# Performance work log

Measured on AMD Instinct MI355X. Metric: run time of the kernel, lower is better.

## Reference

```python
import jax, jax.numpy as jnp
import numpy as np

N, E, D, DE = 40000, 640000, 128, 64
LAMDA = 0.5
NEG_SLOPE = 0.01  # F.leaky_relu default


def setup_inputs() -> dict:
    key = jax.random.key(0)
    ks = jax.random.split(key, 8)
    node_h = jax.random.normal(ks[0], (N, D), dtype=jnp.float32)
    edge_h = jax.random.normal(ks[1], (E, DE), dtype=jnp.float32)
    src = jax.random.randint(ks[2], (E,), 0, N)
    dst = jax.random.randint(ks[3], (E,), 0, N)
    # parameters (torch Linear layout: [out, in])
    fc_w = jax.random.normal(ks[4], (D, D), dtype=jnp.float32) / np.sqrt(D)
    edge_fc_w = jax.random.normal(ks[5], (DE, DE), dtype=jnp.float32) / np.sqrt(DE)
    edge_fc_b = jax.random.normal(ks[6], (DE,), dtype=jnp.float32) * 0.01
    attn_w = jax.random.normal(ks[7], (1, 2 * D + DE), dtype=jnp.float32) / np.sqrt(2 * D + DE)
    return {"node_h": node_h, "edge_h": edge_h, "src": src, "dst": dst,
            "fc_w": fc_w, "edge_fc_w": edge_fc_w, "edge_fc_b": edge_fc_b, "attn_w": attn_w}


def reference(node_h, edge_h, src, dst, fc_w, edge_fc_w, edge_fc_b, attn_w):
    n = node_h.shape[0]
    z = node_h @ fc_w.T                       # [N, D]
    edge_z = edge_h @ edge_fc_w.T + edge_fc_b  # [E, DE]
    # attn_fc(concat([z_src, z_dst, edge_z])) == z_src@w_s + z_dst@w_d + edge_z@w_e
    w = attn_w[0]
    w_s, w_d, w_e = w[:D], w[D:2 * D], w[2 * D:]
    s_node = z @ w_s                           # [N]
    d_node = z @ w_d                           # [N]
    e = s_node[src] + d_node[dst] + edge_z @ w_e  # [E]
    e = jax.nn.leaky_relu(e, NEG_SLOPE)
    # segment softmax over incoming edges of each dst node
    m = jax.ops.segment_max(e, dst, num_segments=n)          # [N]
    ex = jnp.exp(e - m[dst])                                  # [E]
    denom = jax.ops.segment_sum(ex, dst, num_segments=n)     # [N]
    alpha = ex / denom[dst]                                   # [E]
    h = jax.ops.segment_sum(alpha[:, None] * z[src], dst, num_segments=n)  # [N, D]
    return (1.0 - LAMDA) * node_h + LAMDA * h
```

## Files before the change

### kernel.cpp

```cpp
#include <hip/hip_runtime.h>

#define NNODE 40000
#define NEDGE 640000
#define DD 128
#define DE 64
#define SCAN_NBLK ((NNODE + 255) / 256)

#define NODE_BLOCKS 1024
#define EDGE_BLOCKS 4096
#define FUSED_GRID (NODE_BLOCKS + EDGE_BLOCKS)

typedef float fvec4 __attribute__((ext_vector_type(4)));

__device__ __forceinline__ unsigned short f2bf(float f) {
    union { float f; unsigned int i; } c; c.f = f;
    unsigned int b = c.i;
    return (unsigned short)((b + 0x7fffu + ((b >> 16) & 1u)) >> 16);
}

__global__ __launch_bounds__(256) void fused_a(
        const float* __restrict__ node_h,
        const float* __restrict__ fc_w,
        const float* __restrict__ attw,
        const float* __restrict__ efw,
        const float* __restrict__ efb,
        const float* __restrict__ edge_h,
        unsigned int* __restrict__ z_bf,
        float* __restrict__ s_node,
        float* __restrict__ d_node,
        float* __restrict__ ez,
        int* __restrict__ deg) {
    int t = threadIdx.x;
    int b = blockIdx.x;

    int zi = b * 256 + t;
    if (zi < NNODE) deg[zi] = 0;

    if ((b % 5) != 0) {
        int eb = b - b / 5 - 1;
        __shared__ float v[DE + 1];
        if (t < DE) {
            float acc = 0.f;
            for (int j = 0; j < DE; ++j)
                acc += efw[j * DE + t] * attw[2 * DD + j];
            v[t] = acc;
        } else if (t == DE) {
            float acc = 0.f;
            for (int j = 0; j < DE; ++j)
                acc += efb[j] * attw[2 * DD + j];
            v[DE] = acc;
        }
        __syncthreads();

        int lane = t & 63;
        int wave = t >> 6;
        int sub  = lane & 7;
        const float* vv = &v[8 * sub];
        int ebase = eb * 32 + wave * 8 + (lane >> 3);

        for (int e = ebase; e < NEDGE; e += EDGE_BLOCKS * 32) {
            const fvec4* eh = (const fvec4*)(edge_h + (size_t)e * DE);
            fvec4 u0 = __builtin_nontemporal_load(eh + 2 * sub);
            fvec4 u1 = __builtin_nontemporal_load(eh + 2 * sub + 1);
            float ezv = u0.x * vv[0] + u0.y * vv[1] + u0.z * vv[2] + u0.w * vv[3]
                      + u1.x * vv[4] + u1.y * vv[5] + u1.z * vv[6] + u1.w * vv[7];
            ezv += __shfl_xor(ezv, 1, 64);
            ezv += __shfl_xor(ezv, 2, 64);
            ezv += __shfl_xor(ezv, 4, 64);
            if (sub == 0) ez[e] = ezv + v[DE];
        }
        return;
    }

    int nblk = b / 5;
    int th = t & 127, half = t >> 7;

    float4 wreg[DD / 4];
    const float4* wr = (const float4*)(fc_w + th * DD);
#pragma unroll
    for (int i = 0; i < DD / 4; ++i) wreg[i] = wr[i];
    float ws_att = attw[th];
    float wd_att = attw[DD + th];

    __shared__ float x[2][DD];
    __shared__ float red_s[4], red_d[4];

    for (int nb = nblk * 2; nb < NNODE; nb += NODE_BLOCKS * 2) {
        int n = nb + half;
        __syncthreads();
        x[half][th] = node_h[(size_t)n * DD + th];
        __syncthreads();
        const float4* xv = (const float4*)x[half];
        float acc = 0.f;
#pragma unroll
        for (int i = 0; i < DD / 4; ++i) {
            float4 a = wreg[i];
            float4 bx = xv[i];
            acc += a.x * bx.x + a.y * bx.y + a.z * bx.z + a.w * bx.w;
        }
        float nxt = __shfl_down(acc, 1, 64);
        if ((th & 1) == 0) {
            unsigned int p = (unsigned int)f2bf(acc) |
                             ((unsigned int)f2bf(nxt) << 16);
            z_bf[(size_t)n * (DD / 2) + (th >> 1)] = p;
        }

        float sv = acc * ws_att;
        float dv = acc * wd_att;
#pragma unroll
        for (int off = 32; off > 0; off >>= 1) {
            sv += __shfl_down(sv, off, 64);
            dv += __shfl_down(dv, off, 64);
        }
        int wv = t >> 6;
        if ((t & 63) == 0) { red_s[wv] = sv; red_d[wv] = dv; }
        __syncthreads();
        if (t == 0) {
            s_node[nb]     = red_s[0] + red_s[1];
            d_node[nb]     = red_d[0] + red_d[1];
        }
        if (t == 128) {
            s_node[nb + 1] = red_s[2] + red_s[3];
            d_node[nb + 1] = red_d[2] + red_d[3];
        }
    }
}

__global__ __launch_bounds__(256) void pass1b(
        const int* __restrict__ src,
        const int* __restrict__ dst,
        const float* __restrict__ s_node,
        const float* __restrict__ d_node,
        const float* __restrict__ ez,
        float* __restrict__ ex,
        int* __restrict__ deg) {
    int e = blockIdx.x * 256 + threadIdx.x;
    if (e >= NEDGE) return;
    int s = src[e], d = dst[e];
    float ev = s_node[s] + d_node[d] + ez[e];
    ev = ev > 0.f ? ev : 0.01f * ev;
    ex[e] = __expf(ev);
    atomicAdd(&deg[d], 1);
}

__global__ __launch_bounds__(256) void scan_a(const int* __restrict__ deg,
                                              int* __restrict__ lscan,
                                              int* __restrict__ blocksum) {
    __shared__ int s[256];
    int t = threadIdx.x;
    int idx = blockIdx.x * 256 + t;
    int v = (idx < NNODE) ? deg[idx] : 0;
    s[t] = v;
    __syncthreads();
    for (int off = 1; off < 256; off <<= 1) {
        int add = (t >= off) ? s[t - off] : 0;
        __syncthreads();
        s[t] += add;
        __syncthreads();
    }
    if (idx < NNODE) lscan[idx] = s[t] - v;
    if (t == 255) blocksum[blockIdx.x] = s[255];
}

__global__ __launch_bounds__(256) void scan_c(const int* __restrict__ lscan,
                                              const int* __restrict__ blocksum,
                                              int* __restrict__ rowstart,
                                              int* __restrict__ poscnt) {
    __shared__ int s[256];
    int t = threadIdx.x;
    int v = (t < SCAN_NBLK) ? blocksum[t] : 0;
    s[t] = v;
    __syncthreads();
    for (int off = 1; off < 256; off <<= 1) {
        int add = (t >= off) ? s[t - off] : 0;
        __syncthreads();
        s[t] += add;
        __syncthreads();
    }
    __shared__ int excl[256];
    excl[t] = s[t] - v;
    __syncthreads();

    int idx = blockIdx.x * 256 + t;
    if (idx < NNODE) {
        int r = lscan[idx] + excl[blockIdx.x];
        rowstart[idx] = r;
        poscnt[idx]   = r;
    }
    if (blockIdx.x == 0 && t == 0) rowstart[NNODE] = s[255];
}

__global__ void edge_pass2(const int* __restrict__ src,
                           const int* __restrict__ dst,
                           const float* __restrict__ ex,
                           int* __restrict__ poscnt,
                           int2* __restrict__ se_s) {
    int e = blockIdx.x * blockDim.x + threadIdx.x;
    if (e >= NEDGE) return;
    int d = dst[e];
    int p = atomicAdd(&poscnt[d], 1);
    se_s[p] = make_int2(src[e], __float_as_int(ex[e]));
}

__device__ __forceinline__ void acc8(float* a, uint4 w, float ex) {
    a[0] += ex * __uint_as_float(w.x << 16);
    a[1] += ex * __uint_as_float(w.x & 0xffff0000u);
    a[2] += ex * __uint_as_float(w.y << 16);
    a[3] += ex * __uint_as_float(w.y & 0xffff0000u);
    a[4] += ex * __uint_as_float(w.z << 16);
    a[5] += ex * __uint_as_float(w.z & 0xffff0000u);
    a[6] += ex * __uint_as_float(w.w << 16);
    a[7] += ex * __uint_as_float(w.w & 0xffff0000u);
}

__global__ __launch_bounds__(256) void gather_kernel(
        const float* __restrict__ node_h,
        const uint4* __restrict__ z_bf,
        const int* __restrict__ rowstart,
        const int2* __restrict__ se_s,
        float* __restrict__ out) {
    int wave = threadIdx.x >> 6;
    int lane = threadIdx.x & 63;
    int quarter = lane >> 4;
    int hl = lane & 15;
    int n = blockIdx.x * 4 + wave;
    if (n >= NNODE) return;

    int beg = rowstart[n];
    int end = rowstart[n + 1];

    float a[8] = {0.f, 0.f, 0.f, 0.f, 0.f, 0.f, 0.f, 0.f};
    float den = 0.f;
    int j = beg + quarter;
    for (; j + 12 < end; j += 16) {
        int2 se0 = se_s[j];
        int2 se1 = se_s[j + 4];
        int2 se2 = se_s[j + 8];
        int2 se3 = se_s[j + 12];
        uint4 w0 = z_bf[(size_t)se0.x * 16 + hl];
        uint4 w1 = z_bf[(size_t)se1.x * 16 + hl];
        uint4 w2 = z_bf[(size_t)se2.x * 16 + hl];
        uint4 w3 = z_bf[(size_t)se3.x * 16 + hl];
        float ex0 = __int_as_float(se0.y);
        float ex1 = __int_as_float(se1.y);
        float ex2 = __int_as_float(se2.y);
        float ex3 = __int_as_float(se3.y);
        acc8(a, w0, ex0);
        acc8(a, w1, ex1);
        acc8(a, w2, ex2);
        acc8(a, w3, ex3);
        den += (ex0 + ex1) + (ex2 + ex3);
    }
    for (; j + 4 < end; j += 8) {
        int2 se0 = se_s[j];
        int2 se1 = se_s[j + 4];
        uint4 w0 = z_bf[(size_t)se0.x * 16 + hl];
        uint4 w1 = z_bf[(size_t)se1.x * 16 + hl];
        float ex0 = __int_as_float(se0.y);
        float ex1 = __int_as_float(se1.y);
        acc8(a, w0, ex0);
        acc8(a, w1, ex1);
        den += ex0 + ex1;
    }
    if (j < end) {
        int2 se = se_s[j];
        uint4 w = z_bf[(size_t)se.x * 16 + hl];
        float ex = __int_as_float(se.y);
        acc8(a, w, ex);
        den += ex;
    }

#pragma unroll
    for (int k = 0; k < 8; ++k) {
        a[k] += __shfl_xor(a[k], 16, 64);
        a[k] += __shfl_xor(a[k], 32, 64);
    }
    den += __shfl_xor(den, 16, 64);
    den += __shfl_xor(den, 32, 64);

    if (quarter == 0) {
        float inv = den > 0.f ? 0.5f / den : 0.f;
        size_t o = (size_t)n * (DD / 4) + 2 * hl;
        fvec4 nh0 = ((const fvec4*)node_h)[o];
        fvec4 nh1 = ((const fvec4*)node_h)[o + 1];
        fvec4 r0, r1;
        r0.x = 0.5f * nh0.x + a[0] * inv;
        r0.y = 0.5f * nh0.y + a[1] * inv;
        r0.z = 0.5f * nh0.z + a[2] * inv;
        r0.w = 0.5f * nh0.w + a[3] * inv;
        r1.x = 0.5f * nh1.x + a[4] * inv;
        r1.y = 0.5f * nh1.y + a[5] * inv;
        r1.z = 0.5f * nh1.z + a[6] * inv;
        r1.w = 0.5f * nh1.w + a[7] * inv;
        __builtin_nontemporal_store(r0, (fvec4*)out + o);
        __builtin_nontemporal_store(r1, (fvec4*)out + o + 1);
    }
}

extern "C" void kernel_launch(void* const* d_in, const int* in_sizes, int n_in,
                              void* d_out, int out_size, void* d_ws, size_t ws_size,
                              hipStream_t stream) {
    const float* node_h    = (const float*)d_in[0];
    const float* edge_h    = (const float*)d_in[1];
    const int*   src       = (const int*)d_in[2];
    const int*   dst       = (const int*)d_in[3];
    const float* fc_w      = (const float*)d_in[4];
    const float* edge_fc_w = (const float*)d_in[5];
    const float* edge_fc_b = (const float*)d_in[6];
    const float* attn_w    = (const float*)d_in[7];
    float* out = (float*)d_out;

    char* ws = (char*)d_ws;
    unsigned int* z_bf = (unsigned int*)ws;
    int2*  se_s     = (int2*)(ws + (size_t)NNODE * 64 * 4);
    float* s_node   = (float*)(se_s + NEDGE);
    float* d_node   = s_node + NNODE;
    float* ez       = d_node + NNODE;
    float* ex       = ez + NEDGE;
    int*   deg      = (int*)(ex + NEDGE);
    int*   lscan    = deg + NNODE;
    int*   blocksum = lscan + NNODE;
    int*   rowstart = blocksum + 256;
    int*   poscnt   = rowstart + NNODE + 1;

    fused_a<<<FUSED_GRID, 256, 0, stream>>>(node_h, fc_w, attn_w, edge_fc_w,
                                            edge_fc_b, edge_h, z_bf, s_node,
                                            d_node, ez, deg);
    pass1b<<<(NEDGE + 255) / 256, 256, 0, stream>>>(src, dst, s_node, d_node,
                                                    ez, ex, deg);
    scan_a<<<SCAN_NBLK, 256, 0, stream>>>(deg, lscan, blocksum);
    scan_c<<<SCAN_NBLK, 256, 0, stream>>>(lscan, blocksum, rowstart, poscnt);
    edge_pass2<<<NEDGE / 256, 256, 0, stream>>>(src, dst, ex, poscnt, se_s);
    gather_kernel<<<NNODE / 4, 256, 0, stream>>>(node_h, (const uint4*)z_bf,
                                                 rowstart, se_s, out);
}
```

Measured before the change: 420.5 us.

## Split fused node/edge kernel, fold degree count and exp into edge passes

Replaces the interleaved node/edge fused kernel with a dedicated node projection kernel (128 threads, two nodes per iteration) and a separate edge-projection kernel. The edge kernel also does the degree atomics. The leaky-relu/exp score computation moves into the scatter pass, removing the separate pass1b kernel and the intermediate ex array round trip. In exchange, node and edge work no longer overlap within one launch, and the scatter pass now does random gathers of s_node/d_node before its atomics.

```diff
diff --git a/kernel.cpp b/kernel.cpp
--- a/kernel.cpp
+++ b/kernel.cpp
@@ -6,10 +6,6 @@
 #define DE 64
 #define SCAN_NBLK ((NNODE + 255) / 256)
 
-#define NODE_BLOCKS 1024
-#define EDGE_BLOCKS 4096
-#define FUSED_GRID (NODE_BLOCKS + EDGE_BLOCKS)
-
 typedef float fvec4 __attribute__((ext_vector_type(4)));
 
 __device__ __forceinline__ unsigned short f2bf(float f) {
@@ -18,129 +14,141 @@
     return (unsigned short)((b + 0x7fffu + ((b >> 16) & 1u)) >> 16);
 }
 
-__global__ __launch_bounds__(256) void fused_a(
+__global__ __launch_bounds__(128) void node_z(
         const float* __restrict__ node_h,
         const float* __restrict__ fc_w,
         const float* __restrict__ attw,
         const float* __restrict__ efw,
         const float* __restrict__ efb,
-        const float* __restrict__ edge_h,
         unsigned int* __restrict__ z_bf,
         float* __restrict__ s_node,
         float* __restrict__ d_node,
-        float* __restrict__ ez,
+        float* __restrict__ vc,
         int* __restrict__ deg) {
     int t = threadIdx.x;
-    int b = blockIdx.x;
-
-    int zi = b * 256 + t;
+
+    int zi = blockIdx.x * 128 + t;
     if (zi < NNODE) deg[zi] = 0;
 
-    if ((b % 5) != 0) {
-        int eb = b - b / 5 - 1;
-        __shared__ float v[DE + 1];
+    if (blockIdx.x == 0) {
         if (t < DE) {
             float acc = 0.f;
             for (int j = 0; j < DE; ++j)
                 acc += efw[j * DE + t] * attw[2 * DD + j];
-            v[t] = acc;
-        } else if (t == DE) {
+            vc[t] = acc;
+        }
+        if (t == 0) {
             float acc = 0.f;
             for (int j = 0; j < DE; ++j)
                 acc += efb[j] * attw[2 * DD + j];
-            v[DE] = acc;
-        }
-        __syncthreads();
-
-        int lane = t & 63;
-        int wave = t >> 6;
-        int sub  = lane & 7;
-        const float* vv = &v[8 * sub];
-        int ebase = eb * 32 + wave * 8 + (lane >> 3);
-
-        for (int e = ebase; e < NEDGE; e += EDGE_BLOCKS * 32) {
-            const fvec4* eh = (const fvec4*)(edge_h + (size_t)e * DE);
-            fvec4 u0 = __builtin_nontemporal_load(eh + 2 * sub);
-            fvec4 u1 = __builtin_nontemporal_load(eh + 2 * sub + 1);
-            float ezv = u0.x * vv[0] + u0.y * vv[1] + u0.z * vv[2] + u0.w * vv[3]
-                      + u1.x * vv[4] + u1.y * vv[5] + u1.z * vv[6] + u1.w * vv[7];
-            ezv += __shfl_xor(ezv, 1, 64);
-            ezv += __shfl_xor(ezv, 2, 64);
-            ezv += __shfl_xor(ezv, 4, 64);
-            if (sub == 0) ez[e] = ezv + v[DE];
-        }
-        return;
-    }
-
-    int nblk = b / 5;
-    int th = t & 127, half = t >> 7;
+            vc[DE] = acc;
+        }
+    }
 
     float4 wreg[DD / 4];
-    const float4* wr = (const float4*)(fc_w + th * DD);
+    const float4* wr = (const float4*)(fc_w + t * DD);
 #pragma unroll
     for (int i = 0; i < DD / 4; ++i) wreg[i] = wr[i];
-    float ws_att = attw[th];
-    float wd_att = attw[DD + th];
-
-    __shared__ float x[2][DD];
-    __shared__ float red_s[4], red_d[4];
-
-    for (int nb = nblk * 2; nb < NNODE; nb += NODE_BLOCKS * 2) {
-        int n = nb + half;
-        __syncthreads();
-        x[half][th] = node_h[(size_t)n * DD + th];
-        __syncthreads();
-        const float4* xv = (const float4*)x[half];
-        float acc = 0.f;
+    float ws_att = attw[t];
+    float wd_att = attw[DD + t];
+
+    __shared__ float x0[DD], x1[DD];
+    __shared__ float red[4][2];
+
+    for (int nb = blockIdx.x * 2; nb < NNODE; nb += 2048) {
+        __syncthreads();
+        x0[t] = node_h[(size_t)nb * DD + t];
+        x1[t] = node_h[(size_t)(nb + 1) * DD + t];
+        __syncthreads();
+        const float4* xv0 = (const float4*)x0;
+        const float4* xv1 = (const float4*)x1;
+        float acc0 = 0.f, acc1 = 0.f;
 #pragma unroll
         for (int i = 0; i < DD / 4; ++i) {
             float4 a = wreg[i];
-            float4 bx = xv[i];
-            acc += a.x * bx.x + a.y * bx.y + a.z * bx.z + a.w * bx.w;
-        }
-        float nxt = __shfl_down(acc, 1, 64);
-        if ((th & 1) == 0) {
-            unsigned int p = (unsigned int)f2bf(acc) |
-                             ((unsigned int)f2bf(nxt) << 16);
-            z_bf[(size_t)n * (DD / 2) + (th >> 1)] = p;
-        }
-
-        float sv = acc * ws_att;
-        float dv = acc * wd_att;
+            float4 b0 = xv0[i];
+            float4 b1 = xv1[i];
+            acc0 += a.x * b0.x + a.y * b0.y + a.z * b0.z + a.w * b0.w;
+            acc1 += a.x * b1.x + a.y * b1.y + a.z * b1.z + a.w * b1.w;
+        }
+        float nxt0 = __shfl_down(acc0, 1, 64);
+        float nxt1 = __shfl_down(acc1, 1, 64);
+        if ((t & 1) == 0) {
+            unsigned int p0 = (unsigned int)f2bf(acc0) |
+                              ((unsigned int)f2bf(nxt0) << 16);
+            unsigned int p1 = (unsigned int)f2bf(acc1) |
+                              ((unsigned int)f2bf(nxt1) << 16);
+            z_bf[(size_t)nb * (DD / 2) + (t >> 1)]       = p0;
+            z_bf[(size_t)(nb + 1) * (DD / 2) + (t >> 1)] = p1;
+        }
+
+        float s0 = acc0 * ws_att, d0 = acc0 * wd_att;
+        float s1 = acc1 * ws_att, d1 = acc1 * wd_att;
 #pragma unroll
         for (int off = 32; off > 0; off >>= 1) {
-            sv += __shfl_down(sv, off, 64);
-            dv += __shfl_down(dv, off, 64);
+            s0 += __shfl_down(s0, off, 64);
+            d0 += __shfl_down(d0, off, 64);
+            s1 += __shfl_down(s1, off, 64);
+            d1 += __shfl_down(d1, off, 64);
         }
         int wv = t >> 6;
-        if ((t & 63) == 0) { red_s[wv] = sv; red_d[wv] = dv; }
+        if ((t & 63) == 0) {
+            red[0][wv] = s0; red[1][wv] = d0;
+            red[2][wv] = s1; red[3][wv] = d1;
+        }
         __syncthreads();
         if (t == 0) {
-            s_node[nb]     = red_s[0] + red_s[1];
-            d_node[nb]     = red_d[0] + red_d[1];
-        }
-        if (t == 128) {
-            s_node[nb + 1] = red_s[2] + red_s[3];
-            d_node[nb + 1] = red_d[2] + red_d[3];
-        }
-    }
-}
-
-__global__ __launch_bounds__(256) void pass1b(
-        const int* __restrict__ src,
+            s_node[nb]     = red[0][0] + red[0][1];
+            d_node[nb]     = red[1][0] + red[1][1];
+            s_node[nb + 1] = red[2][0] + red[2][1];
+            d_node[nb + 1] = red[3][0] + red[3][1];
+        }
+    }
+}
+
+__global__ __launch_bounds__(256) void edge_ez(
+        const float* __restrict__ edge_h,
+        const float* __restrict__ vc,
         const int* __restrict__ dst,
-        const float* __restrict__ s_node,
-        const float* __restrict__ d_node,
-        const float* __restrict__ ez,
-        float* __restrict__ ex,
+        float* __restrict__ ez,
         int* __restrict__ deg) {
-    int e = blockIdx.x * 256 + threadIdx.x;
-    if (e >= NEDGE) return;
-    int s = src[e], d = dst[e];
-    float ev = s_node[s] + d_node[d] + ez[e];
-    ev = ev > 0.f ? ev : 0.01f * ev;
-    ex[e] = __expf(ev);
-    atomicAdd(&deg[d], 1);
+    __shared__ float v[DE + 1];
+    int t = threadIdx.x;
+    if (t <= DE) v[t] = vc[t];
+    __syncthreads();
+
+    int lane = t & 63;
+    int wave = t >> 6;
+    int sub  = lane & 3;
+    int eslot = lane >> 2;
+    int e0 = blockIdx.x * 128 + wave * 32 + eslot;
+    int e1 = e0 + 16;
+
+    const fvec4* eh0 = (const fvec4*)(edge_h + (size_t)e0 * DE) + sub * 4;
+    const fvec4* eh1 = (const fvec4*)(edge_h + (size_t)e1 * DE) + sub * 4;
+    fvec4 a0 = eh0[0], a1 = eh0[1], a2 = eh0[2], a3 = eh0[3];
+    fvec4 b0 = eh1[0], b1 = eh1[1], b2 = eh1[2], b3 = eh1[3];
+
+    const float* vv = &v[16 * sub];
+    float d0 = a0.x * vv[0]  + a0.y * vv[1]  + a0.z * vv[2]  + a0.w * vv[3]
+             + a1.x * vv[4]  + a1.y * vv[5]  + a1.z * vv[6]  + a1.w * vv[7]
+             + a2.x * vv[8]  + a2.y * vv[9]  + a2.z * vv[10] + a2.w * vv[11]
+             + a3.x * vv[12] + a3.y * vv[13] + a3.z * vv[14] + a3.w * vv[15];
+    float d1 = b0.x * vv[0]  + b0.y * vv[1]  + b0.z * vv[2]  + b0.w * vv[3]
+             + b1.x * vv[4]  + b1.y * vv[5]  + b1.z * vv[6]  + b1.w * vv[7]
+             + b2.x * vv[8]  + b2.y * vv[9]  + b2.z * vv[10] + b2.w * vv[11]
+             + b3.x * vv[12] + b3.y * vv[13] + b3.z * vv[14] + b3.w * vv[15];
+    d0 += __shfl_xor(d0, 1, 64);
+    d0 += __shfl_xor(d0, 2, 64);
+    d1 += __shfl_xor(d1, 1, 64);
+    d1 += __shfl_xor(d1, 2, 64);
+
+    if (sub == 0) {
+        ez[e0] = d0 + v[DE];
+        ez[e1] = d1 + v[DE];
+        atomicAdd(&deg[dst[e0]], 1);
+        atomicAdd(&deg[dst[e1]], 1);
+    }
 }
 
 __global__ __launch_bounds__(256) void scan_a(const int* __restrict__ deg,
@@ -190,16 +198,22 @@
     if (blockIdx.x == 0 && t == 0) rowstart[NNODE] = s[255];
 }
 
-__global__ void edge_pass2(const int* __restrict__ src,
-                           const int* __restrict__ dst,
-                           const float* __restrict__ ex,
-                           int* __restrict__ poscnt,
-                           int2* __restrict__ se_s) {
-    int e = blockIdx.x * blockDim.x + threadIdx.x;
+__global__ __launch_bounds__(256) void pass12(
+        const int* __restrict__ src,
+        const int* __restrict__ dst,
+        const float* __restrict__ s_node,
+        const float* __restrict__ d_node,
+        const float* __restrict__ ez,
+        int* __restrict__ poscnt,
+        int2* __restrict__ se_s) {
+    int e = blockIdx.x * 256 + threadIdx.x;
     if (e >= NEDGE) return;
-    int d = dst[e];
+    int s = src[e], d = dst[e];
+    float ev = s_node[s] + d_node[d] + ez[e];
+    ev = ev > 0.f ? ev : 0.01f * ev;
+    float ex = __expf(ev);
     int p = atomicAdd(&poscnt[d], 1);
-    se_s[p] = make_int2(src[e], __float_as_int(ex[e]));
+    se_s[p] = make_int2(s, __float_as_int(ex));
 }
 
 __device__ __forceinline__ void acc8(float* a, uint4 w, float ex) {
@@ -315,22 +329,21 @@
     int2*  se_s     = (int2*)(ws + (size_t)NNODE * 64 * 4);
     float* s_node   = (float*)(se_s + NEDGE);
     float* d_node   = s_node + NNODE;
-    float* ez       = d_node + NNODE;
-    float* ex       = ez + NEDGE;
-    int*   deg      = (int*)(ex + NEDGE);
+    float* vc       = d_node + NNODE;
+    float* ez       = vc + 128;
+    int*   deg      = (int*)(ez + NEDGE);
     int*   lscan    = deg + NNODE;
     int*   blocksum = lscan + NNODE;
     int*   rowstart = blocksum + 256;
     int*   poscnt   = rowstart + NNODE + 1;
 
-    fused_a<<<FUSED_GRID, 256, 0, stream>>>(node_h, fc_w, attn_w, edge_fc_w,
-                                            edge_fc_b, edge_h, z_bf, s_node,
-                                            d_node, ez, deg);
-    pass1b<<<(NEDGE + 255) / 256, 256, 0, stream>>>(src, dst, s_node, d_node,
-                                                    ez, ex, deg);
+    node_z<<<1024, 128, 0, stream>>>(node_h, fc_w, attn_w, edge_fc_w,
+                                     edge_fc_b, z_bf, s_node, d_node, vc, deg);
+    edge_ez<<<NEDGE / 128, 256, 0, stream>>>(edge_h, vc, dst, ez, deg);
     scan_a<<<SCAN_NBLK, 256, 0, stream>>>(deg, lscan, blocksum);
     scan_c<<<SCAN_NBLK, 256, 0, stream>>>(lscan, blocksum, rowstart, poscnt);
-    edge_pass2<<<NEDGE / 256, 256, 0, stream>>>(src, dst, ex, poscnt, se_s);
+    pass12<<<(NEDGE + 255) / 256, 256, 0, stream>>>(src, dst, s_node, d_node,
+                                                    ez, poscnt, se_s);
     gather_kernel<<<NNODE / 4, 256, 0, stream>>>(node_h, (const uint4*)z_bf,
                                                  rowstart, se_s, out);
 }
```

Measured after the change: 388.4 us. -7.7%, faster.
